# Kernel tuning notes

Measured on AMD Instinct MI355X. Metric: run time of the kernel, lower is better.

Reference implementation:

```python
import jax, jax.numpy as jnp
import numpy as np

EPS = 1e-5        # BatchNorm eps (torch default)
SLOPE = 0.2       # LeakyReLU negative slope
K_DIL, K_DIL_POS, K = 8, 6, 32


def _sqdist(a):
    # a: (B,N,D) -> squared pairwise distances (B,N,N); monotone in cdist(p=2)
    n = jnp.sum(a * a, axis=-1)
    return n[:, :, None] + n[:, None, :] - 2.0 * jnp.einsum('bnd,bmd->bnm', a, a)


def _knn(a, k):
    # k nearest neighbors excluding self (drop the closest = self, as in torch topk[..., 1:])
    _, idx = jax.lax.top_k(-_sqdist(a), k + 1)
    return idx[:, :, 1:]  # (B,N,k) int32


def _edge_feat(x, idx):
    # x: (B,N,C), idx: (B,N,K) -> (B,N,K,2C) = concat(neighbor - center, center)
    B = x.shape[0]
    b_idx = jnp.arange(B)[:, None, None]
    nbr = x[b_idx, idx]                       # (B,N,K,C) gather
    ctr = x[:, :, None, :]                    # (B,N,1,C)
    ctr_b = jnp.broadcast_to(ctr, nbr.shape)
    return jnp.concatenate([nbr - ctr, ctr_b], axis=-1)


def _conv_bn_lrelu(f, W, g, b):
    # 1x1 Conv2d (no bias) + BatchNorm2d(track_running_stats=False, batch stats) + LeakyReLU(0.2)
    # f: (B,N,K,Cin), W: (Cout,Cin)
    y = jnp.einsum('bnkc,oc->bnko', f, W)
    mu = jnp.mean(y, axis=(0, 1, 2))
    var = jnp.var(y, axis=(0, 1, 2))          # biased var, as torch BN normalization
    y = (y - mu) * jax.lax.rsqrt(var + EPS) * g + b
    return jnp.where(y > 0, y, SLOPE * y)


def setup_inputs() -> dict:
    key = jax.random.key(0)
    ks = jax.random.split(key, 8)
    B, N, C, D = 2, 4096, 64, 3
    hidden, out_c = 128, 64
    c1 = 2 * C   # convdilated channels
    c2 = 4 * C   # conv input channels (edge feature of 2C-dim features)
    return {
        'x': jax.random.normal(ks[0], (B, N, C), jnp.float32),
        'pos': jax.random.normal(ks[1], (B, N, D), jnp.float32),
        'W1': jax.random.normal(ks[2], (c1, c1), jnp.float32) * 0.05,
        'g1': jnp.ones((c1,), jnp.float32),
        'b1': jnp.zeros((c1,), jnp.float32),
        'W2': jax.random.normal(ks[3], (hidden, c2), jnp.float32) * 0.05,
        'g2': jnp.ones((hidden,), jnp.float32),
        'b2': jnp.zeros((hidden,), jnp.float32),
        'W3': jax.random.normal(ks[4], (out_c, hidden), jnp.float32) * 0.05,
        'g3': jnp.ones((out_c,), jnp.float32),
        'b3': jnp.zeros((out_c,), jnp.float32),
    }


def reference(x, pos, W1, g1, b1, W2, g2, b2, W3, g3, b3):
    # Dual graph 1: feature-KNN (k_dilated) concat pos-KNN (k_dilated_pos)
    idx1 = jnp.concatenate([_knn(x, K_DIL), _knn(pos, K_DIL_POS)], axis=2)  # (B,N,14)
    f1 = _edge_feat(x, idx1)                                                # (B,N,14,2C)
    h1 = jnp.max(_conv_bn_lrelu(f1, W1, g1, b1), axis=2)                    # (B,N,2C)
    # Graph 2: k_pos == 0 -> pure position KNN
    idx2 = _knn(pos, K)                                                     # (B,N,32)
    f2 = _edge_feat(h1, idx2)                                               # (B,N,32,4C)
    h2 = _conv_bn_lrelu(f2, W2, g2, b2)                                     # (B,N,32,hidden)
    h3 = _conv_bn_lrelu(h2, W3, g3, b3)                                     # (B,N,32,out)
    out = jnp.max(h3, axis=2)                                               # (B,N,out)
    return out, idx2
```

## Files before the change

### kernel.cpp

```cpp
#include <hip/hip_runtime.h>
#include <hip/hip_bf16.h>
#include <type_traits>

using bf16 = __hip_bfloat16;

namespace {

constexpr int B_ = 2;
constexpr int N_ = 4096;
constexpr int C_ = 64;
constexpr int K14_ = 14;
constexpr int KX_ = 8;
constexpr int KP_ = 6;
constexpr int K2_ = 32;
constexpr int OC_ = 64;

__device__ __forceinline__ float bflo(unsigned u) { return __uint_as_float(u << 16); }
__device__ __forceinline__ float bfhi(unsigned u) { return __uint_as_float(u & 0xffff0000u); }

__device__ __forceinline__ unsigned pack_f16(float a, float b) {
  _Float16 ha = (_Float16)a, hb = (_Float16)b;
  unsigned short ua = __builtin_bit_cast(unsigned short, ha);
  unsigned short ub = __builtin_bit_cast(unsigned short, hb);
  return (unsigned)ua | ((unsigned)ub << 16);
}

using half2v = __attribute__((ext_vector_type(2))) _Float16;
__device__ __forceinline__ float dot2(unsigned a, unsigned b, float acc) {
#if __has_builtin(__builtin_amdgcn_fdot2)
  return __builtin_amdgcn_fdot2(__builtin_bit_cast(half2v, a),
                                __builtin_bit_cast(half2v, b), acc, false);
#else
  half2v ha = __builtin_bit_cast(half2v, a), hb = __builtin_bit_cast(half2v, b);
  acc = fmaf((float)ha[0], (float)hb[0], acc);
  return fmaf((float)ha[1], (float)hb[1], acc);
#endif
}

__device__ __forceinline__ unsigned fmono(float d) {
  unsigned u = __float_as_uint(d);
  return u ^ (((int)u < 0) ? 0xFFFFFFFFu : 0x80000000u);
}

#define GRP8_ONE(GV, GS, T) \
  { bool av = !((taken >> (T)) & 1ull); bool bb = av && dst[T] < GV; \
    GV = bb ? dst[T] : GV; GS = bb ? (T) : GS; }
#define GRP8(GV, GS, B) do { GV = 3.0e38f; GS = B; \
  GRP8_ONE(GV, GS, (B)+0) GRP8_ONE(GV, GS, (B)+1) GRP8_ONE(GV, GS, (B)+2) \
  GRP8_ONE(GV, GS, (B)+3) GRP8_ONE(GV, GS, (B)+4) GRP8_ONE(GV, GS, (B)+5) \
  GRP8_ONE(GV, GS, (B)+6) GRP8_ONE(GV, GS, (B)+7) } while (0)
#define GTREE_ONE(GV, GS) { bool bb = GV < pv; pv = bb ? GV : pv; ptt = bb ? GS : ptt; }
#define GTREE() do { pv = gv0; ptt = gs0; \
  GTREE_ONE(gv1, gs1) GTREE_ONE(gv2, gs2) GTREE_ONE(gv3, gs3) GTREE_ONE(gv4, gs4) \
  GTREE_ONE(gv5, gs5) GTREE_ONE(gv6, gs6) GTREE_ONE(gv7, gs7) } while (0)
#define GRP_SWITCH(TT) do { switch ((TT) >> 3) { \
  case 0: GRP8(gv0, gs0, 0);  break; case 1: GRP8(gv1, gs1, 8);  break; \
  case 2: GRP8(gv2, gs2, 16); break; case 3: GRP8(gv3, gs3, 24); break; \
  case 4: GRP8(gv4, gs4, 32); break; case 5: GRP8(gv5, gs5, 40); break; \
  case 6: GRP8(gv6, gs6, 48); break; case 7: GRP8(gv7, gs7, 56); break; } \
  GTREE(); } while (0)
#define SEL_DECL float gv0, gv1, gv2, gv3, gv4, gv5, gv6, gv7; \
  int gs0, gs1, gs2, gs3, gs4, gs5, gs6, gs7; float pv; int ptt; \
  unsigned long long taken = 0ull;
#define SEL_INIT do { \
  GRP8(gv0, gs0, 0);  GRP8(gv1, gs1, 8);  GRP8(gv2, gs2, 16); GRP8(gv3, gs3, 24); \
  GRP8(gv4, gs4, 32); GRP8(gv5, gs5, 40); GRP8(gv6, gs6, 48); GRP8(gv7, gs7, 56); \
  GTREE(); } while (0)

__global__ __launch_bounds__(256)
void xnorm_kernel(const float* __restrict__ x, float* __restrict__ nx)
{
  int p = blockIdx.x * 256 + threadIdx.x;
  if (p >= B_ * N_) return;
  float s = 0.f;
#pragma unroll 8
  for (int c = 0; c < C_; ++c) { float v = x[p * C_ + c]; s = fmaf(v, v, s); }
  nx[p] = s;
}

__global__ __launch_bounds__(256)
void wprep_kernel(const float* __restrict__ W1, const float* __restrict__ W2,
                  const float* __restrict__ W3,
                  float* __restrict__ WT1a, float* __restrict__ WT1bm,
                  float* __restrict__ WT2a, float* __restrict__ WT2bm,
                  unsigned* __restrict__ w3p)
{
  int idx = blockIdx.x * 256 + threadIdx.x;
  if (idx < 128 * 128) {
    int o = idx & 127, c = idx >> 7;
    float a = W2[o * 256 + c];
    WT2a[c * 128 + o] = a;
    WT2bm[c * 128 + o] = W2[o * 256 + 128 + c] - a;
    if (c < 64) {
      float a1 = W1[o * 128 + c];
      WT1a[c * 128 + o] = a1;
      WT1bm[c * 128 + o] = W1[o * 128 + 64 + c] - a1;
    }
  }
  if (idx < 64 * 64) {
    int oo = idx & 63, c2 = idx >> 6;
    w3p[c2 * 64 + oo] = pack_f16(W3[oo * 128 + 2 * c2], W3[oo * 128 + 2 * c2 + 1]);
  }
}

__global__ __launch_bounds__(512, 4)
void knn_x_kernel(const float* __restrict__ x, const float* __restrict__ nx,
                  int* __restrict__ idx1)
{
  __shared__ unsigned tileh[256 * 33];
  const int wave = threadIdx.x >> 6, lane = threadIdx.x & 63;
  const int qg = blockIdx.x * 8 + wave;
  const int bb = qg >> 12;
  const float* xb = x + bb * N_ * C_;
  unsigned myq;
  {
    float2 qv = *(const float2*)&x[qg * C_ + 2 * (lane & 31)];
    myq = pack_f16(qv.x, qv.y);
  }
  unsigned qp[32];
#pragma unroll
  for (int c2 = 0; c2 < 32; ++c2) qp[c2] = __builtin_amdgcn_readlane(myq, c2);
  const float nq = nx[qg];
  const float* nb_ = nx + bb * N_;
  float dst[64];
#pragma unroll
  for (int ti = 0; ti < 16; ++ti) {
    __syncthreads();
    for (int e = threadIdx.x; e < 256 * 32; e += 512) {
      int c2 = e & 31, j = e >> 5;
      float2 v = *(const float2*)&xb[(ti * 256 + j) * C_ + 2 * c2];
      tileh[j * 33 + c2] = pack_f16(v.x, v.y);
    }
    __syncthreads();
#pragma unroll
    for (int nb4 = 0; nb4 < 4; ++nb4) {
      const unsigned* row = &tileh[(nb4 * 64 + lane) * 33];
      float acc = 0.f;
#pragma unroll
      for (int c2 = 0; c2 < 32; ++c2) acc = dot2(qp[c2], row[c2], acc);
      float nbv = nb_[ti * 256 + nb4 * 64 + lane];
      dst[ti * 4 + nb4] = nq + nbv - 2.f * acc;
    }
  }
  SEL_DECL;
  SEL_INIT;
  for (int r = 0; r < KX_ + 1; ++r) {
    int j = ((ptt >> 2) << 8) + ((ptt & 3) << 6) + lane;
    unsigned long long key = ((unsigned long long)fmono(pv) << 32) | (unsigned)j;
#pragma unroll
    for (int m = 1; m < 64; m <<= 1) {
      unsigned long long ok = __shfl_xor(key, m, 64);
      key = ok < key ? ok : key;
    }
    int wj = (int)(key & 0xFFFFFFFFull);
    if (r > 0 && lane == 0) idx1[qg * K14_ + (r - 1)] = wj;
    if ((wj & 63) == lane) {
      int tt = ((wj >> 8) << 2) | ((wj >> 6) & 3);
      taken |= 1ull << tt;
      GRP_SWITCH(tt);
    }
  }
}

__global__ __launch_bounds__(512, 2)
void knn_pos_kernel(const float* __restrict__ pos,
                    int* __restrict__ idx1, int* __restrict__ idx2,
                    float* __restrict__ oidx)
{
#pragma clang fp contract(off)
  __shared__ float pL[3][N_];
  __shared__ float nL[N_];
  const int wave = threadIdx.x >> 6, lane = threadIdx.x & 63;
  const int qg = blockIdx.x * 8 + wave;
  const int bb = qg >> 12;
  const float* pb = pos + bb * N_ * 3;
  for (int j = threadIdx.x; j < N_; j += 512) {
    float a = pb[j * 3], b = pb[j * 3 + 1], c = pb[j * 3 + 2];
    pL[0][j] = a; pL[1][j] = b; pL[2][j] = c;
    float aa = a * a;
    float bb2 = b * b;
    float cc = c * c;
    float s1 = aa + bb2;
    nL[j] = s1 + cc;
  }
  __syncthreads();
  const int q = qg & (N_ - 1);
  const float qx = pL[0][q], qy = pL[1][q], qz = pL[2][q];
  const float nq = nL[q];
  float dst[64];
#pragma unroll
  for (int t = 0; t < 64; ++t) {
    int j = t * 64 + lane;
    float dot = qx * pL[0][j];
    dot = fmaf(qy, pL[1][j], dot);
    dot = fmaf(qz, pL[2][j], dot);
    float t1 = nq + nL[j];
    float t2 = 2.0f * dot;
    dst[t] = t1 - t2;
  }
  SEL_DECL;
  SEL_INIT;
  for (int r = 0; r < K2_ + 1; ++r) {
    int j = ptt * 64 + lane;
    unsigned long long key = ((unsigned long long)fmono(pv) << 32) | (unsigned)j;
#pragma unroll
    for (int m = 1; m < 64; m <<= 1) {
      unsigned long long ok = __shfl_xor(key, m, 64);
      key = ok < key ? ok : key;
    }
    int wj = (int)(key & 0xFFFFFFFFull);
    if (r > 0 && lane == 0) {
      int rr = r - 1;
      if (rr < KP_) idx1[qg * K14_ + KX_ + rr] = wj;
      idx2[qg * K2_ + rr] = wj;
      oidx[qg * K2_ + rr] = (float)wj;
    }
    if ((wj & 63) == lane) {
      int tt = wj >> 6;
      taken |= 1ull << tt;
      GRP_SWITCH(tt);
    }
  }
}

template<int CIN, typename TIN>
__global__ __launch_bounds__(256)
void lin_kernel(const TIN* __restrict__ in, const float* __restrict__ WT,
                bf16* __restrict__ out)
{
  __shared__ float wt[CIN * 128];
  for (int e = threadIdx.x; e < CIN * 128; e += 256) wt[e] = WT[e];
  __syncthreads();
  const int which = threadIdx.x >> 7, o = threadIdx.x & 127;
  for (int p0 = blockIdx.x * 2; p0 < B_ * N_; p0 += gridDim.x * 2) {
    int p = p0 + which;
    float acc = 0.f;
#pragma unroll 8
    for (int c = 0; c < CIN; ++c) {
      float v;
      if constexpr (std::is_same_v<TIN, float>) v = in[p * CIN + c];
      else v = __bfloat162float(in[p * CIN + c]);
      acc = fmaf(wt[c * 128 + o], v, acc);
    }
    out[p * 128 + o] = __float2bfloat16(acc);
  }
}

template<int KNB>
__global__ __launch_bounds__(256)
void stats_gather_kernel(const bf16* __restrict__ a, const bf16* __restrict__ ac,
                         const int* __restrict__ nbr, double* __restrict__ st)
{
  const int o = threadIdx.x & 127;
  const int which = threadIdx.x >> 7;
  double s = 0.0, s2 = 0.0;
  for (int p0 = blockIdx.x * 2; p0 < B_ * N_; p0 += gridDim.x * 2) {
    int p = p0 + which;
    int base = (p >> 12) << 12;
    float acv = __bfloat162float(ac[p * 128 + o]);
#pragma unroll 2
    for (int kk = 0; kk < KNB; ++kk) {
      int nb = nbr[p * KNB + kk] & (N_ - 1);
      float y = __bfloat162float(a[(base + nb) * 128 + o]) + acv;
      s += (double)y; s2 += (double)y * (double)y;
    }
  }
  atomicAdd(&st[o], s);
  atomicAdd(&st[128 + o], s2);
}

__global__ void bnfin_kernel(const double* __restrict__ st, const float* __restrict__ g,
                             const float* __restrict__ bi, float* __restrict__ so,
                             int nch, double cnt)
{
  int o = threadIdx.x;
  if (o >= nch) return;
  double mu = st[o] / cnt;
  double var = st[nch + o] / cnt - mu * mu;
  double sc = (double)g[o] / sqrt(var + 1e-5);
  so[o] = (float)sc;
  so[nch + o] = (float)((double)bi[o] - mu * sc);
}

__global__ __launch_bounds__(256)
void h1_kernel(const bf16* __restrict__ u, const bf16* __restrict__ uc,
               const int* __restrict__ idx1, const float* __restrict__ so,
               bf16* __restrict__ h1)
{
  const int o = threadIdx.x & 127, which = threadIdx.x >> 7;
  float sc = so[o], off = so[128 + o];
  for (int p0 = blockIdx.x * 2; p0 < B_ * N_; p0 += gridDim.x * 2) {
    int p = p0 + which;
    int base = (p >> 12) << 12;
    float ucv = __bfloat162float(uc[p * 128 + o]);
    float m = -3.0e38f;
#pragma unroll
    for (int kk = 0; kk < K14_; ++kk) {
      int nb = idx1[p * K14_ + kk] & (N_ - 1);
      float y = __bfloat162float(u[(base + nb) * 128 + o]) + ucv;
      float v = fmaf(y, sc, off);
      v = v > 0.f ? v : 0.2f * v;
      m = fmaxf(m, v);
    }
    h1[p * 128 + o] = __float2bfloat16(m);
  }
}

__global__ __launch_bounds__(256, 5)
void conv3s_kernel(const bf16* __restrict__ z, const bf16* __restrict__ zc,
                   const int* __restrict__ idx2, const float* __restrict__ so2,
                   const unsigned* __restrict__ w3p,
                   double* __restrict__ st3, unsigned* __restrict__ y3m)
{
  __shared__ unsigned w3s[64 * 64];
  __shared__ unsigned h2s[4][512];
  {
    const uint4* src = (const uint4*)w3p;
    uint4* dst4 = (uint4*)w3s;
    for (int e = threadIdx.x; e < 1024; e += 256) dst4[e] = src[e];
  }
  __syncthreads();
  const int wave = threadIdx.x >> 6, lane = threadIdx.x & 63;
  unsigned* h2w = &h2s[wave][0];
  const int swz = (lane >> 2) & 7;
  const float sclo = so2[2 * lane],       schi = so2[2 * lane + 1];
  const float offlo = so2[128 + 2 * lane], offhi = so2[129 + 2 * lane];
  double s = 0.0, s2 = 0.0;
  const int gw = blockIdx.x * 4 + wave;
  const int stride = gridDim.x * 4;
  for (int p = gw; p < B_ * N_; p += stride) {
    const int base = (p >> 12) << 12;
    const unsigned zcv = *(const unsigned*)&zc[p * 128 + 2 * lane];
    const float zclo = bflo(zcv), zchi = bfhi(zcv);
    float mx = -3.0e38f, mn = 3.0e38f;
#pragma unroll
    for (int kc = 0; kc < 4; ++kc) {
      asm volatile("s_waitcnt lgkmcnt(0)" ::: "memory");
#pragma unroll
      for (int i = 0; i < 8; ++i) {
        int nb = idx2[p * K2_ + kc * 8 + i] & (N_ - 1);
        unsigned zv = *(const unsigned*)&z[(base + nb) * 128 + 2 * lane];
        float y0 = bflo(zv) + zclo;
        float y1 = bfhi(zv) + zchi;
        float v0 = fmaf(y0, sclo, offlo); v0 = v0 > 0.f ? v0 : 0.2f * v0;
        float v1 = fmaf(y1, schi, offhi); v1 = v1 > 0.f ? v1 : 0.2f * v1;
        h2w[(lane << 3) | (i ^ swz)] = pack_f16(v0, v1);
      }
      asm volatile("s_waitcnt lgkmcnt(0)" ::: "memory");
      float a0 = 0.f, a1 = 0.f, a2 = 0.f, a3 = 0.f;
      float a4 = 0.f, a5 = 0.f, a6 = 0.f, a7 = 0.f;
#pragma unroll
      for (int c2 = 0; c2 < 64; ++c2) {
        const int cs = (c2 >> 2) & 7;
        unsigned wp = w3s[(c2 << 6) | lane];
        uint4 ra = *(const uint4*)&h2w[c2 << 3];
        uint4 rb = *(const uint4*)&h2w[(c2 << 3) + 4];
        unsigned hv[8] = {ra.x, ra.y, ra.z, ra.w, rb.x, rb.y, rb.z, rb.w};
        a0 = dot2(wp, hv[0 ^ cs], a0);
        a1 = dot2(wp, hv[1 ^ cs], a1);
        a2 = dot2(wp, hv[2 ^ cs], a2);
        a3 = dot2(wp, hv[3 ^ cs], a3);
        a4 = dot2(wp, hv[4 ^ cs], a4);
        a5 = dot2(wp, hv[5 ^ cs], a5);
        a6 = dot2(wp, hv[6 ^ cs], a6);
        a7 = dot2(wp, hv[7 ^ cs], a7);
      }
      s += (double)a0 + (double)a1 + (double)a2 + (double)a3
         + (double)a4 + (double)a5 + (double)a6 + (double)a7;
      s2 += (double)a0 * a0 + (double)a1 * a1 + (double)a2 * a2 + (double)a3 * a3
          + (double)a4 * a4 + (double)a5 * a5 + (double)a6 * a6 + (double)a7 * a7;
      mx = fmaxf(mx, fmaxf(fmaxf(a0, a1), fmaxf(a2, a3)));
      mx = fmaxf(mx, fmaxf(fmaxf(a4, a5), fmaxf(a6, a7)));
      mn = fminf(mn, fminf(fminf(a0, a1), fminf(a2, a3)));
      mn = fminf(mn, fminf(fminf(a4, a5), fminf(a6, a7)));
    }
    y3m[p * OC_ + lane] = pack_f16(mx, mn);
  }
  atomicAdd(&st3[lane], s);
  atomicAdd(&st3[64 + lane], s2);
}

__global__ __launch_bounds__(256)
void fin3_kernel(const unsigned* __restrict__ y3m, const float* __restrict__ so3,
                 float* __restrict__ outp)
{
  int idx = blockIdx.x * 256 + threadIdx.x;
  if (idx >= B_ * N_ * OC_) return;
  int oo = idx & 63;
  float sc3 = so3[oo], off3 = so3[64 + oo];
  half2v hv = __builtin_bit_cast(half2v, y3m[idx]);
  float pick = (sc3 >= 0.f) ? (float)hv[0] : (float)hv[1];
  float v = fmaf(pick, sc3, off3);
  outp[idx] = v > 0.f ? v : 0.2f * v;
}

}

extern "C" void kernel_launch(void* const* d_in, const int* in_sizes, int n_in,
                              void* d_out, int out_size, void* d_ws, size_t ws_size,
                              hipStream_t stream) {
  const float* x   = (const float*)d_in[0];
  const float* pos = (const float*)d_in[1];
  const float* W1  = (const float*)d_in[2];
  const float* g1  = (const float*)d_in[3];
  const float* b1  = (const float*)d_in[4];
  const float* W2  = (const float*)d_in[5];
  const float* g2  = (const float*)d_in[6];
  const float* b2  = (const float*)d_in[7];
  const float* W3  = (const float*)d_in[8];
  const float* g3  = (const float*)d_in[9];
  const float* b3  = (const float*)d_in[10];

  float* outp = (float*)d_out;
  float* oidx = outp + B_ * N_ * OC_;

  char* w = (char*)d_ws;
  double* stats = (double*)w;            w += 640 * sizeof(double);
  float* nxf    = (float*)w;             w += B_ * N_ * 4;
  float* WT1a   = (float*)w;             w += 64 * 128 * 4;
  float* WT1bm  = (float*)w;             w += 64 * 128 * 4;
  float* WT2a   = (float*)w;             w += 128 * 128 * 4;
  float* WT2bm  = (float*)w;             w += 128 * 128 * 4;
  unsigned* w3p = (unsigned*)w;          w += 64 * 64 * 4;
  float* so1    = (float*)w;             w += 256 * 4;
  float* so2    = (float*)w;             w += 256 * 4;
  float* so3    = (float*)w;             w += 128 * 4;
  int* idx1     = (int*)w;               w += B_ * N_ * K14_ * 4;
  int* idx2i    = (int*)w;               w += B_ * N_ * K2_ * 4;
  bf16* u       = (bf16*)w;              w += B_ * N_ * 128 * 2;
  bf16* uc      = (bf16*)w;              w += B_ * N_ * 128 * 2;
  bf16* h1      = (bf16*)w;              w += B_ * N_ * 128 * 2;
  bf16* zz  = u;
  bf16* zzc = uc;
  unsigned* y3m = (unsigned*)h1;

  hipMemsetAsync(stats, 0, 640 * sizeof(double), stream);

  xnorm_kernel<<<(B_ * N_ + 255) / 256, 256, 0, stream>>>(x, nxf);
  wprep_kernel<<<64, 256, 0, stream>>>(W1, W2, W3, WT1a, WT1bm, WT2a, WT2bm, w3p);

  knn_x_kernel<<<1024, 512, 0, stream>>>(x, nxf, idx1);
  knn_pos_kernel<<<1024, 512, 0, stream>>>(pos, idx1, idx2i, oidx);

  lin_kernel<64, float><<<2048, 256, 0, stream>>>(x, WT1a, u);
  lin_kernel<64, float><<<2048, 256, 0, stream>>>(x, WT1bm, uc);

  stats_gather_kernel<K14_><<<2048, 256, 0, stream>>>(u, uc, idx1, stats);
  bnfin_kernel<<<1, 128, 0, stream>>>(stats, g1, b1, so1, 128, (double)(B_ * N_ * K14_));
  h1_kernel<<<2048, 256, 0, stream>>>(u, uc, idx1, so1, h1);

  lin_kernel<128, bf16><<<2048, 256, 0, stream>>>(h1, WT2a, zz);
  lin_kernel<128, bf16><<<2048, 256, 0, stream>>>(h1, WT2bm, zzc);

  stats_gather_kernel<K2_><<<2048, 256, 0, stream>>>(zz, zzc, idx2i, stats + 256);
  bnfin_kernel<<<1, 128, 0, stream>>>(stats + 256, g2, b2, so2, 128, (double)(B_ * N_ * K2_));

  conv3s_kernel<<<1024, 256, 0, stream>>>(zz, zzc, idx2i, so2, w3p, stats + 512, y3m);
  bnfin_kernel<<<1, 128, 0, stream>>>(stats + 512, g3, b3, so3, 64, (double)(B_ * N_ * K2_));
  fin3_kernel<<<B_ * N_ * OC_ / 256, 256, 0, stream>>>(y3m, so3, outp);
}
```

Measured before the change: 698.6 us.

## Use fp32 transposed tiles in feature KNN and prefetch gathers in conv3

The feature-KNN distance kernel drops the packed fp16 dot2 path and computes fp32 FMAs against a channel-major transposed shared tile of 128 points. This raises precision of neighbor selection but doubles FMA work and tile passes. Separately, conv3s now prefetches the next group of neighbor gathers into registers while the current group is processed, to hide global latency, and its grid size is doubled.

```diff
diff --git a/kernel.cpp b/kernel.cpp
--- a/kernel.cpp
+++ b/kernel.cpp
@@ -107,45 +107,50 @@
 void knn_x_kernel(const float* __restrict__ x, const float* __restrict__ nx,
                   int* __restrict__ idx1)
 {
-  __shared__ unsigned tileh[256 * 33];
+  __shared__ float tile[C_ * 129];
   const int wave = threadIdx.x >> 6, lane = threadIdx.x & 63;
   const int qg = blockIdx.x * 8 + wave;
   const int bb = qg >> 12;
   const float* xb = x + bb * N_ * C_;
-  unsigned myq;
-  {
-    float2 qv = *(const float2*)&x[qg * C_ + 2 * (lane & 31)];
-    myq = pack_f16(qv.x, qv.y);
-  }
-  unsigned qp[32];
-#pragma unroll
-  for (int c2 = 0; c2 < 32; ++c2) qp[c2] = __builtin_amdgcn_readlane(myq, c2);
+  float myq = x[qg * C_ + lane];
+  float qs[64];
+#pragma unroll
+  for (int c = 0; c < 64; ++c)
+    qs[c] = __uint_as_float(__builtin_amdgcn_readlane(__float_as_uint(myq), c));
   const float nq = nx[qg];
   const float* nb_ = nx + bb * N_;
+  const int jst = threadIdx.x >> 4;
+  const int cst = (threadIdx.x & 15) * 4;
   float dst[64];
 #pragma unroll
-  for (int ti = 0; ti < 16; ++ti) {
+  for (int ti = 0; ti < 32; ++ti) {
     __syncthreads();
-    for (int e = threadIdx.x; e < 256 * 32; e += 512) {
-      int c2 = e & 31, j = e >> 5;
-      float2 v = *(const float2*)&xb[(ti * 256 + j) * C_ + 2 * c2];
-      tileh[j * 33 + c2] = pack_f16(v.x, v.y);
+#pragma unroll
+    for (int i = 0; i < 4; ++i) {
+      int j = jst + 32 * i;
+      float4 v = *(const float4*)&xb[(ti * 128 + j) * C_ + cst];
+      tile[(cst + 0) * 129 + j] = v.x;
+      tile[(cst + 1) * 129 + j] = v.y;
+      tile[(cst + 2) * 129 + j] = v.z;
+      tile[(cst + 3) * 129 + j] = v.w;
     }
     __syncthreads();
-#pragma unroll
-    for (int nb4 = 0; nb4 < 4; ++nb4) {
-      const unsigned* row = &tileh[(nb4 * 64 + lane) * 33];
-      float acc = 0.f;
-#pragma unroll
-      for (int c2 = 0; c2 < 32; ++c2) acc = dot2(qp[c2], row[c2], acc);
-      float nbv = nb_[ti * 256 + nb4 * 64 + lane];
-      dst[ti * 4 + nb4] = nq + nbv - 2.f * acc;
-    }
+    float n0 = nb_[ti * 128 + lane];
+    float n1 = nb_[ti * 128 + 64 + lane];
+    const float* t0 = &tile[lane];
+    float a0 = 0.f, a1 = 0.f;
+#pragma unroll
+    for (int c = 0; c < 64; ++c) {
+      a0 = fmaf(qs[c], t0[c * 129], a0);
+      a1 = fmaf(qs[c], t0[c * 129 + 64], a1);
+    }
+    dst[ti * 2 + 0] = nq + n0 - 2.f * a0;
+    dst[ti * 2 + 1] = nq + n1 - 2.f * a1;
   }
   SEL_DECL;
   SEL_INIT;
   for (int r = 0; r < KX_ + 1; ++r) {
-    int j = ((ptt >> 2) << 8) + ((ptt & 3) << 6) + lane;
+    int j = ptt * 64 + lane;
     unsigned long long key = ((unsigned long long)fmono(pv) << 32) | (unsigned)j;
 #pragma unroll
     for (int m = 1; m < 64; m <<= 1) {
@@ -155,7 +160,7 @@
     int wj = (int)(key & 0xFFFFFFFFull);
     if (r > 0 && lane == 0) idx1[qg * K14_ + (r - 1)] = wj;
     if ((wj & 63) == lane) {
-      int tt = ((wj >> 8) << 2) | ((wj >> 6) & 3);
+      int tt = wj >> 6;
       taken |= 1ull << tt;
       GRP_SWITCH(tt);
     }
@@ -330,21 +335,33 @@
   const int stride = gridDim.x * 4;
   for (int p = gw; p < B_ * N_; p += stride) {
     const int base = (p >> 12) << 12;
+    const int* idxp = &idx2[p * K2_];
     const unsigned zcv = *(const unsigned*)&zc[p * 128 + 2 * lane];
     const float zclo = bflo(zcv), zchi = bfhi(zcv);
+    unsigned zv[8];
+#pragma unroll
+    for (int i = 0; i < 8; ++i) {
+      int nb = idxp[i] & (N_ - 1);
+      zv[i] = *(const unsigned*)&z[(base + nb) * 128 + 2 * lane];
+    }
     float mx = -3.0e38f, mn = 3.0e38f;
 #pragma unroll
     for (int kc = 0; kc < 4; ++kc) {
       asm volatile("s_waitcnt lgkmcnt(0)" ::: "memory");
 #pragma unroll
       for (int i = 0; i < 8; ++i) {
-        int nb = idx2[p * K2_ + kc * 8 + i] & (N_ - 1);
-        unsigned zv = *(const unsigned*)&z[(base + nb) * 128 + 2 * lane];
-        float y0 = bflo(zv) + zclo;
-        float y1 = bfhi(zv) + zchi;
+        float y0 = bflo(zv[i]) + zclo;
+        float y1 = bfhi(zv[i]) + zchi;
         float v0 = fmaf(y0, sclo, offlo); v0 = v0 > 0.f ? v0 : 0.2f * v0;
         float v1 = fmaf(y1, schi, offhi); v1 = v1 > 0.f ? v1 : 0.2f * v1;
         h2w[(lane << 3) | (i ^ swz)] = pack_f16(v0, v1);
+      }
+      if (kc < 3) {
+#pragma unroll
+        for (int i = 0; i < 8; ++i) {
+          int nb = idxp[(kc + 1) * 8 + i] & (N_ - 1);
+          zv[i] = *(const unsigned*)&z[(base + nb) * 128 + 2 * lane];
+        }
       }
       asm volatile("s_waitcnt lgkmcnt(0)" ::: "memory");
       float a0 = 0.f, a1 = 0.f, a2 = 0.f, a3 = 0.f;
@@ -455,7 +472,7 @@
   stats_gather_kernel<K2_><<<2048, 256, 0, stream>>>(zz, zzc, idx2i, stats + 256);
   bnfin_kernel<<<1, 128, 0, stream>>>(stats + 256, g2, b2, so2, 128, (double)(B_ * N_ * K2_));
 
-  conv3s_kernel<<<1024, 256, 0, stream>>>(zz, zzc, idx2i, so2, w3p, stats + 512, y3m);
+  conv3s_kernel<<<2048, 256, 0, stream>>>(zz, zzc, idx2i, so2, w3p, stats + 512, y3m);
   bnfin_kernel<<<1, 128, 0, stream>>>(stats + 512, g3, b3, so3, 64, (double)(B_ * N_ * K2_));
   fin3_kernel<<<B_ * N_ * OC_ / 256, 256, 0, stream>>>(y3m, so3, outp);
 }
```

Measured after the change: 1.716 ms. 146% more time.

## Shrink KNN blocks to 256 threads and prefetch neighbor rows in conv3s

Applied to the files above, without the earlier changes.

Both KNN kernels now launch 256-thread blocks handling 4 queries each, with twice as many blocks. This changes occupancy and tile-load amortisation: the knn_x tile is now reloaded by fewer waves per block, and knn_pos reloads the whole 4096-point position set for every 4 queries instead of 8. conv3s now software-pipelines its neighbor gathers, issuing loads for the next 8 neighbors before the W3 dot-product loop so global latency overlaps compute, and it launches twice as many blocks. A DSTV macro hook is added to the selection macros but expands to the same array access.

```diff
diff --git a/kernel.cpp b/kernel.cpp
--- a/kernel.cpp
+++ b/kernel.cpp
@@ -43,8 +43,8 @@
 }
 
 #define GRP8_ONE(GV, GS, T) \
-  { bool av = !((taken >> (T)) & 1ull); bool bb = av && dst[T] < GV; \
-    GV = bb ? dst[T] : GV; GS = bb ? (T) : GS; }
+  { bool av = !((taken >> (T)) & 1ull); float dv_ = DSTV(T); bool bb = av && dv_ < GV; \
+    GV = bb ? dv_ : GV; GS = bb ? (T) : GS; }
 #define GRP8(GV, GS, B) do { GV = 3.0e38f; GS = B; \
   GRP8_ONE(GV, GS, (B)+0) GRP8_ONE(GV, GS, (B)+1) GRP8_ONE(GV, GS, (B)+2) \
   GRP8_ONE(GV, GS, (B)+3) GRP8_ONE(GV, GS, (B)+4) GRP8_ONE(GV, GS, (B)+5) \
@@ -103,13 +103,13 @@
   }
 }
 
-__global__ __launch_bounds__(512, 4)
+__global__ __launch_bounds__(256)
 void knn_x_kernel(const float* __restrict__ x, const float* __restrict__ nx,
                   int* __restrict__ idx1)
 {
   __shared__ unsigned tileh[256 * 33];
   const int wave = threadIdx.x >> 6, lane = threadIdx.x & 63;
-  const int qg = blockIdx.x * 8 + wave;
+  const int qg = blockIdx.x * 4 + wave;
   const int bb = qg >> 12;
   const float* xb = x + bb * N_ * C_;
   unsigned myq;
@@ -126,7 +126,7 @@
 #pragma unroll
   for (int ti = 0; ti < 16; ++ti) {
     __syncthreads();
-    for (int e = threadIdx.x; e < 256 * 32; e += 512) {
+    for (int e = threadIdx.x; e < 256 * 32; e += 256) {
       int c2 = e & 31, j = e >> 5;
       float2 v = *(const float2*)&xb[(ti * 256 + j) * C_ + 2 * c2];
       tileh[j * 33 + c2] = pack_f16(v.x, v.y);
@@ -142,6 +142,7 @@
       dst[ti * 4 + nb4] = nq + nbv - 2.f * acc;
     }
   }
+#define DSTV(T) dst[T]
   SEL_DECL;
   SEL_INIT;
   for (int r = 0; r < KX_ + 1; ++r) {
@@ -160,9 +161,10 @@
       GRP_SWITCH(tt);
     }
   }
-}
-
-__global__ __launch_bounds__(512, 2)
+#undef DSTV
+}
+
+__global__ __launch_bounds__(256)
 void knn_pos_kernel(const float* __restrict__ pos,
                     int* __restrict__ idx1, int* __restrict__ idx2,
                     float* __restrict__ oidx)
@@ -171,10 +173,10 @@
   __shared__ float pL[3][N_];
   __shared__ float nL[N_];
   const int wave = threadIdx.x >> 6, lane = threadIdx.x & 63;
-  const int qg = blockIdx.x * 8 + wave;
+  const int qg = blockIdx.x * 4 + wave;
   const int bb = qg >> 12;
   const float* pb = pos + bb * N_ * 3;
-  for (int j = threadIdx.x; j < N_; j += 512) {
+  for (int j = threadIdx.x; j < N_; j += 256) {
     float a = pb[j * 3], b = pb[j * 3 + 1], c = pb[j * 3 + 2];
     pL[0][j] = a; pL[1][j] = b; pL[2][j] = c;
     float aa = a * a;
@@ -198,6 +200,7 @@
     float t2 = 2.0f * dot;
     dst[t] = t1 - t2;
   }
+#define DSTV(T) dst[T]
   SEL_DECL;
   SEL_INIT;
   for (int r = 0; r < K2_ + 1; ++r) {
@@ -221,6 +224,7 @@
       GRP_SWITCH(tt);
     }
   }
+#undef DSTV
 }
 
 template<int CIN, typename TIN>
@@ -330,21 +334,33 @@
   const int stride = gridDim.x * 4;
   for (int p = gw; p < B_ * N_; p += stride) {
     const int base = (p >> 12) << 12;
+    const int* idxp = &idx2[p * K2_];
     const unsigned zcv = *(const unsigned*)&zc[p * 128 + 2 * lane];
     const float zclo = bflo(zcv), zchi = bfhi(zcv);
+    unsigned zv[8];
+#pragma unroll
+    for (int i = 0; i < 8; ++i) {
+      int nb = idxp[i] & (N_ - 1);
+      zv[i] = *(const unsigned*)&z[(base + nb) * 128 + 2 * lane];
+    }
     float mx = -3.0e38f, mn = 3.0e38f;
 #pragma unroll
     for (int kc = 0; kc < 4; ++kc) {
       asm volatile("s_waitcnt lgkmcnt(0)" ::: "memory");
 #pragma unroll
       for (int i = 0; i < 8; ++i) {
-        int nb = idx2[p * K2_ + kc * 8 + i] & (N_ - 1);
-        unsigned zv = *(const unsigned*)&z[(base + nb) * 128 + 2 * lane];
-        float y0 = bflo(zv) + zclo;
-        float y1 = bfhi(zv) + zchi;
+        float y0 = bflo(zv[i]) + zclo;
+        float y1 = bfhi(zv[i]) + zchi;
         float v0 = fmaf(y0, sclo, offlo); v0 = v0 > 0.f ? v0 : 0.2f * v0;
         float v1 = fmaf(y1, schi, offhi); v1 = v1 > 0.f ? v1 : 0.2f * v1;
         h2w[(lane << 3) | (i ^ swz)] = pack_f16(v0, v1);
+      }
+      if (kc < 3) {
+#pragma unroll
+        for (int i = 0; i < 8; ++i) {
+          int nb = idxp[(kc + 1) * 8 + i] & (N_ - 1);
+          zv[i] = *(const unsigned*)&z[(base + nb) * 128 + 2 * lane];
+        }
       }
       asm volatile("s_waitcnt lgkmcnt(0)" ::: "memory");
       float a0 = 0.f, a1 = 0.f, a2 = 0.f, a3 = 0.f;
@@ -439,8 +455,8 @@
   xnorm_kernel<<<(B_ * N_ + 255) / 256, 256, 0, stream>>>(x, nxf);
   wprep_kernel<<<64, 256, 0, stream>>>(W1, W2, W3, WT1a, WT1bm, WT2a, WT2bm, w3p);
 
-  knn_x_kernel<<<1024, 512, 0, stream>>>(x, nxf, idx1);
-  knn_pos_kernel<<<1024, 512, 0, stream>>>(pos, idx1, idx2i, oidx);
+  knn_x_kernel<<<2048, 256, 0, stream>>>(x, nxf, idx1);
+  knn_pos_kernel<<<2048, 256, 0, stream>>>(pos, idx1, idx2i, oidx);
 
   lin_kernel<64, float><<<2048, 256, 0, stream>>>(x, WT1a, u);
   lin_kernel<64, float><<<2048, 256, 0, stream>>>(x, WT1bm, uc);
@@ -455,7 +471,7 @@
   stats_gather_kernel<K2_><<<2048, 256, 0, stream>>>(zz, zzc, idx2i, stats + 256);
   bnfin_kernel<<<1, 128, 0, stream>>>(stats + 256, g2, b2, so2, 128, (double)(B_ * N_ * K2_));
 
-  conv3s_kernel<<<1024, 256, 0, stream>>>(zz, zzc, idx2i, so2, w3p, stats + 512, y3m);
+  conv3s_kernel<<<2048, 256, 0, stream>>>(zz, zzc, idx2i, so2, w3p, stats + 512, y3m);
   bnfin_kernel<<<1, 128, 0, stream>>>(stats + 512, g3, b3, so3, 64, (double)(B_ * N_ * K2_));
   fin3_kernel<<<B_ * N_ * OC_ / 256, 256, 0, stream>>>(y3m, so3, outp);
 }
```

Result: slower. 864.2 us (+23.7%).
